# Kernel tuning notes

Hardware: AMD Instinct MI355X
Metric: run time of the kernel (lower is better)

## Reference

```python
import jax, jax.numpy as jnp
import numpy as np

D_MODEL = 1024
N_HEADS = 16
D_K = D_MODEL // N_HEADS
THETA = 10000.0
MAX_SEQ_LEN = 2048


def _rope_tables(seq_len):
    pos = jnp.arange(seq_len, dtype=jnp.float32)
    inv_freq = 1.0 / (THETA ** (jnp.arange(0, D_K, 2, dtype=jnp.float32) / D_K))
    ang = pos[:, None] * inv_freq[None, :]  # [T, D_K/2]
    return jnp.cos(ang), jnp.sin(ang)


def _apply_rope(x, cos, sin):
    # x: [..., T, D_K]; cos/sin: [T, D_K/2]
    x_even = x[..., ::2]
    x_odd = x[..., 1::2]
    r_even = x_even * cos - x_odd * sin
    r_odd = x_even * sin + x_odd * cos
    out = jnp.stack([r_even, r_odd], axis=-1)  # [..., T, D_K/2, 2]
    return out.reshape(x.shape)


def setup_inputs() -> dict:
    key = jax.random.key(0)
    ks = jax.random.split(key, 5)
    std = np.sqrt(2.0 / (D_MODEL + D_MODEL))
    x = jax.random.normal(ks[0], (2, 2048, D_MODEL), dtype=jnp.float32)
    w_q = jax.random.normal(ks[1], (D_MODEL, D_MODEL), dtype=jnp.float32) * std
    w_k = jax.random.normal(ks[2], (D_MODEL, D_MODEL), dtype=jnp.float32) * std
    w_v = jax.random.normal(ks[3], (D_MODEL, D_MODEL), dtype=jnp.float32) * std
    w_o = jax.random.normal(ks[4], (D_MODEL, D_MODEL), dtype=jnp.float32) * std
    return {"x": x, "w_q": w_q, "w_k": w_k, "w_v": w_v, "w_o": w_o}


def reference(x, w_q, w_k, w_v, w_o):
    B, T, _ = x.shape
    # projections: weight stored as [d_out, d_in], y = x @ W^T
    q = jnp.einsum('btd,od->bto', x, w_q)
    k = jnp.einsum('btd,od->bto', x, w_k)
    v = jnp.einsum('btd,od->bto', x, w_v)
    # split heads: [B, T, H*Dk] -> [B, H, T, Dk]
    q = q.reshape(B, T, N_HEADS, D_K).transpose(0, 2, 1, 3)
    k = k.reshape(B, T, N_HEADS, D_K).transpose(0, 2, 1, 3)
    v = v.reshape(B, T, N_HEADS, D_K).transpose(0, 2, 1, 3)
    cos, sin = _rope_tables(T)
    q = _apply_rope(q, cos, sin)
    k = _apply_rope(k, cos, sin)
    scores = jnp.einsum('bhqd,bhkd->bhqk', q, k) / np.sqrt(D_K).astype(np.float32)
    causal = jnp.tril(jnp.ones((T, T), dtype=bool))
    scores = jnp.where(causal, scores, -jnp.inf)
    attn = jax.nn.softmax(scores, axis=-1)
    out = jnp.einsum('bhqk,bhkd->bhqd', attn, v)
    out = out.transpose(0, 2, 1, 3).reshape(B, T, D_MODEL)
    return jnp.einsum('btd,od->bto', out, w_o)
```

## Files before the change

### kernel.cpp

```cpp
#include <hip/hip_runtime.h>
#include <hip/hip_bf16.h>

typedef __bf16 bf16_t;
typedef __bf16 bf16x8 __attribute__((ext_vector_type(8)));
typedef float f32x4 __attribute__((ext_vector_type(4)));
typedef short short4v __attribute__((ext_vector_type(4)));

#define D_MODEL 1024
#define T_SEQ 2048
#define NH 16
#define DKD 64
#define X_ELEMS (4194304u)
#define W_ELEMS (1048576u)
#define Q_SCALE 0.18033688011112042f

__device__ __forceinline__ void async16(const bf16_t* g, bf16_t* l) {
    __builtin_amdgcn_global_load_lds((const __attribute__((address_space(1))) void*)g,
                                     (__attribute__((address_space(3))) void*)l, 16, 0, 0);
}

__global__ __launch_bounds__(256) void convert_kernel(
    const float* __restrict__ x, const float* __restrict__ wq,
    const float* __restrict__ wk, const float* __restrict__ wv,
    const float* __restrict__ wo,
    bf16_t* __restrict__ xb, bf16_t* __restrict__ wqb, bf16_t* __restrict__ wkb,
    bf16_t* __restrict__ wvb, bf16_t* __restrict__ wob)
{
    size_t idx = ((size_t)blockIdx.x * 256 + threadIdx.x) * 4;
    const float* src; bf16_t* dst; size_t off;
    if (idx < X_ELEMS) { src = x; dst = xb; off = idx; }
    else {
        size_t r = idx - X_ELEMS;
        unsigned w = (unsigned)(r >> 20);
        off = r & (W_ELEMS - 1);
        src = (w == 0) ? wq : (w == 1) ? wk : (w == 2) ? wv : wo;
        dst = (w == 0) ? wqb : (w == 1) ? wkb : (w == 2) ? wvb : wob;
    }
    float4 v = *(const float4*)(src + off);
    union { bf16_t b[4]; short4v s; } u;
    u.b[0] = (bf16_t)v.x; u.b[1] = (bf16_t)v.y;
    u.b[2] = (bf16_t)v.z; u.b[3] = (bf16_t)v.w;
    *(short4v*)(dst + off) = u.s;
}

__global__ __launch_bounds__(256) void rope_kernel(float* __restrict__ cost, float* __restrict__ sint)
{
    int idx = blockIdx.x * 256 + threadIdx.x;
    int t = idx >> 5, i = idx & 31;
    float inv = expf(-0.28782313662425572f * (float)i);
    float ang = (float)t * inv;
    float s, c;
    sincosf(ang, &s, &c);
    cost[idx] = c; sint[idx] = s;
}

__global__ __launch_bounds__(256) void gemm_fused(
    const bf16_t* __restrict__ A,
    const bf16_t* __restrict__ W0, const bf16_t* __restrict__ W1, const bf16_t* __restrict__ W2,
    bf16_t* __restrict__ qout, bf16_t* __restrict__ kout, bf16_t* __restrict__ vout,
    const float* __restrict__ cost, const float* __restrict__ sint,
    float* __restrict__ fout, int modeBase)
{
    const int K = 1024;
    __shared__ bf16_t As[128 * 32];
    __shared__ bf16_t Bs[128 * 32];
    const int tid = threadIdx.x;
    const int wave = tid >> 6, lane = tid & 63;
    const int quad = lane >> 4, l16 = lane & 15;
    const int m0 = blockIdx.x * 128;
    const int n0 = blockIdx.y * 128;
    const int wm = (wave >> 1) * 64, wn = (wave & 1) * 64;
    const int mode = modeBase + blockIdx.z;
    const bf16_t* W = (mode == 1) ? W1 : (mode == 2) ? W2 : W0;

    const bf16_t* Afrag = (mode == 2) ? Bs : As;
    const bf16_t* Bfrag = (mode == 2) ? As : Bs;
    const int aoff = (mode == 2) ? wn : wm;
    const int boff = (mode == 2) ? wm : wn;

    const f32x4 fzero = {0.f, 0.f, 0.f, 0.f};
    f32x4 acc[4][4];
    #pragma unroll
    for (int i = 0; i < 4; ++i)
        #pragma unroll
        for (int j = 0; j < 4; ++j) acc[i][j] = fzero;

    for (int k0 = 0; k0 < K; k0 += 32) {
        __syncthreads();
        #pragma unroll
        for (int c = 0; c < 2; ++c) {
            int G = c * 256 + tid;
            int row = G >> 2, go = G & 3;
            async16(A + (size_t)(m0 + row) * K + (k0 + go * 8), As + (size_t)(c * 256 + wave * 64) * 8);
            async16(W + (size_t)(n0 + row) * K + (k0 + go * 8), Bs + (size_t)(c * 256 + wave * 64) * 8);
        }
        __syncthreads();
        bf16x8 af[4], bfv[4];
        #pragma unroll
        for (int mi = 0; mi < 4; ++mi)
            af[mi] = *(const bf16x8*)(Afrag + (aoff + mi * 16 + l16) * 32 + quad * 8);
        #pragma unroll
        for (int ni = 0; ni < 4; ++ni)
            bfv[ni] = *(const bf16x8*)(Bfrag + (boff + ni * 16 + l16) * 32 + quad * 8);
        #pragma unroll
        for (int mi = 0; mi < 4; ++mi)
            #pragma unroll
            for (int ni = 0; ni < 4; ++ni)
                acc[mi][ni] = __builtin_amdgcn_mfma_f32_16x16x32_bf16(af[mi], bfv[ni], acc[mi][ni], 0, 0, 0);
    }

    #pragma unroll
    for (int mi = 0; mi < 4; ++mi) {
        #pragma unroll
        for (int ni = 0; ni < 4; ++ni) {
            #pragma unroll
            for (int reg = 0; reg < 4; ++reg) {
                float v = acc[mi][ni][reg];
                if (mode == 2) {
                    int f   = n0 + wn + mi * 16 + quad * 4 + reg;
                    int tok = m0 + wm + ni * 16 + l16;
                    int t = tok & (T_SEQ - 1), b = tok >> 11;
                    int h = f >> 6, dk = f & 63;
                    vout[(((size_t)b * NH + h) * DKD + dk) * T_SEQ + t] = (bf16_t)v;
                } else {
                    int row = m0 + wm + mi * 16 + quad * 4 + reg;
                    int col = n0 + wn + ni * 16 + l16;
                    if (mode == 3) {
                        fout[(size_t)row * D_MODEL + col] = v;
                    } else {
                        int t = row & (T_SEQ - 1), b = row >> 11;
                        int h = col >> 6, dk = col & 63;
                        float vp = __shfl_xor(v, 1);
                        int fi = dk >> 1;
                        float c = cost[t * 32 + fi], s = sint[t * 32 + fi];
                        float r = (dk & 1) ? (vp * s + v * c) : (v * c - vp * s);
                        if (mode == 0) r *= Q_SCALE;
                        bf16_t* dst = (mode == 0) ? qout : kout;
                        dst[(((size_t)b * NH + h) * T_SEQ + t) * DKD + dk] = (bf16_t)r;
                    }
                }
            }
        }
    }
}

__global__ __launch_bounds__(64, 2) void attn_kernel(
    const bf16_t* __restrict__ Q, const bf16_t* __restrict__ Kb,
    const bf16_t* __restrict__ Vt, bf16_t* __restrict__ O)
{
    __shared__ bf16_t Pw[2][16 * 72];
    const int lane = threadIdx.x;
    const int quad = lane >> 4, l16 = lane & 15;
    const int bh = blockIdx.x;
    const int qw = (63 - (int)blockIdx.y) * 32;

    const bf16_t* kbase = Kb + (size_t)bh * T_SEQ * DKD;
    const bf16_t* vbase = Vt + (size_t)bh * DKD * T_SEQ;

    bf16x8 qf[2][2];
    #pragma unroll
    for (int j = 0; j < 2; ++j) {
        const bf16_t* qp = Q + ((size_t)bh * T_SEQ + qw + j * 16 + l16) * DKD;
        qf[j][0] = *(const bf16x8*)(qp + quad * 8);
        qf[j][1] = *(const bf16x8*)(qp + 32 + quad * 8);
    }
    const f32x4 fzero = {0.f, 0.f, 0.f, 0.f};
    f32x4 oacc[2][4];
    #pragma unroll
    for (int j = 0; j < 2; ++j)
        #pragma unroll
        for (int i = 0; i < 4; ++i) oacc[j][i] = fzero;
    float lsum[2] = {0.f, 0.f};

    const int nkt = (qw + 95) >> 6;

    bf16x8 kcur[4][2], knxt[4][2], vcur[4][2];
    #pragma unroll
    for (int fi = 0; fi < 4; ++fi) {
        const bf16_t* kr = kbase + (size_t)(fi * 16 + l16) * DKD + quad * 8;
        kcur[fi][0] = *(const bf16x8*)(kr);
        kcur[fi][1] = *(const bf16x8*)(kr + 32);
    }

    for (int kt = 0; kt < nkt; ++kt) {
        const int k0 = kt * 64;
        #pragma unroll
        for (int di = 0; di < 4; ++di) {
            const bf16_t* vr = vbase + (size_t)(di * 16 + l16) * T_SEQ + k0 + quad * 8;
            vcur[di][0] = *(const bf16x8*)(vr);
            vcur[di][1] = *(const bf16x8*)(vr + 32);
        }
        if (kt + 1 < nkt) {
            #pragma unroll
            for (int fi = 0; fi < 4; ++fi) {
                const bf16_t* kr = kbase + (size_t)(k0 + 64 + fi * 16 + l16) * DKD + quad * 8;
                knxt[fi][0] = *(const bf16x8*)(kr);
                knxt[fi][1] = *(const bf16x8*)(kr + 32);
            }
        }

        #pragma unroll
        for (int j = 0; j < 2; ++j) {
            if (k0 > qw + j * 16 + 15) continue;
            const int qcol = qw + j * 16 + l16;
            f32x4 s[4];
            #pragma unroll
            for (int fi = 0; fi < 4; ++fi) {
                f32x4 z = fzero;
                z = __builtin_amdgcn_mfma_f32_16x16x32_bf16(kcur[fi][0], qf[j][0], z, 0, 0, 0);
                z = __builtin_amdgcn_mfma_f32_16x16x32_bf16(kcur[fi][1], qf[j][1], z, 0, 0, 0);
                s[fi] = z;
            }
            if (k0 + 63 > qw + j * 16) {
                #pragma unroll
                for (int fi = 0; fi < 4; ++fi)
                    #pragma unroll
                    for (int reg = 0; reg < 4; ++reg) {
                        int key = k0 + fi * 16 + quad * 4 + reg;
                        s[fi][reg] = (key > qcol) ? -__builtin_inff() : s[fi][reg];
                    }
            }
            float sm = 0.f;
            #pragma unroll
            for (int fi = 0; fi < 4; ++fi)
                #pragma unroll
                for (int reg = 0; reg < 4; ++reg) {
                    float p = __builtin_amdgcn_exp2f(s[fi][reg]);
                    s[fi][reg] = p;
                    sm += p;
                }
            lsum[j] += sm;

            bf16_t* pw = &Pw[j][0];
            #pragma unroll
            for (int fi = 0; fi < 4; ++fi) {
                union { bf16_t h[4]; unsigned long long u64; } pk;
                pk.h[0] = (bf16_t)s[fi][0]; pk.h[1] = (bf16_t)s[fi][1];
                pk.h[2] = (bf16_t)s[fi][2]; pk.h[3] = (bf16_t)s[fi][3];
                *(unsigned long long*)(pw + l16 * 72 + fi * 16 + quad * 4) = pk.u64;
            }
            bf16x8 pf[2];
            pf[0] = *(const bf16x8*)(pw + l16 * 72 + quad * 8);
            pf[1] = *(const bf16x8*)(pw + l16 * 72 + 32 + quad * 8);

            #pragma unroll
            for (int di = 0; di < 4; ++di) {
                oacc[j][di] = __builtin_amdgcn_mfma_f32_16x16x32_bf16(vcur[di][0], pf[0], oacc[j][di], 0, 0, 0);
                oacc[j][di] = __builtin_amdgcn_mfma_f32_16x16x32_bf16(vcur[di][1], pf[1], oacc[j][di], 0, 0, 0);
            }
        }

        if (kt + 1 < nkt) {
            #pragma unroll
            for (int fi = 0; fi < 4; ++fi) {
                kcur[fi][0] = knxt[fi][0];
                kcur[fi][1] = knxt[fi][1];
            }
        }
    }

    const int b = bh >> 4, h = bh & 15;
    #pragma unroll
    for (int j = 0; j < 2; ++j) {
        float l = lsum[j];
        l += __shfl_xor(l, 16);
        l += __shfl_xor(l, 32);
        float rl = 1.0f / l;
        int q = qw + j * 16 + l16;
        #pragma unroll
        for (int di = 0; di < 4; ++di) {
            union { bf16_t hh[4]; unsigned long long u64; } ok;
            #pragma unroll
            for (int reg = 0; reg < 4; ++reg) ok.hh[reg] = (bf16_t)(oacc[j][di][reg] * rl);
            int d = di * 16 + quad * 4;
            *(unsigned long long*)(O + ((size_t)b * T_SEQ + q) * D_MODEL + h * DKD + d) = ok.u64;
        }
    }
}

extern "C" void kernel_launch(void* const* d_in, const int* in_sizes, int n_in,
                              void* d_out, int out_size, void* d_ws, size_t ws_size,
                              hipStream_t stream)
{
    const float* x  = (const float*)d_in[0];
    const float* wq = (const float*)d_in[1];
    const float* wk = (const float*)d_in[2];
    const float* wv = (const float*)d_in[3];
    const float* wo = (const float*)d_in[4];
    float* out = (float*)d_out;

    char* ws = (char*)d_ws;
    size_t off = 0;
    auto alloc = [&](size_t bytes) -> void* {
        void* p = ws + off; off += (bytes + 255) & ~(size_t)255; return p;
    };
    bf16_t* xb   = (bf16_t*)alloc((size_t)X_ELEMS * 2);
    bf16_t* wqb  = (bf16_t*)alloc((size_t)W_ELEMS * 2);
    bf16_t* wkb  = (bf16_t*)alloc((size_t)W_ELEMS * 2);
    bf16_t* wvb  = (bf16_t*)alloc((size_t)W_ELEMS * 2);
    bf16_t* wob  = (bf16_t*)alloc((size_t)W_ELEMS * 2);
    bf16_t* qb   = (bf16_t*)alloc((size_t)X_ELEMS * 2);
    bf16_t* kb   = (bf16_t*)alloc((size_t)X_ELEMS * 2);
    bf16_t* vtb  = (bf16_t*)alloc((size_t)X_ELEMS * 2);
    bf16_t* ob   = (bf16_t*)alloc((size_t)X_ELEMS * 2);
    float*  cost = (float*)alloc((size_t)T_SEQ * 32 * 4);
    float*  sint = (float*)alloc((size_t)T_SEQ * 32 * 4);

    convert_kernel<<<8192, 256, 0, stream>>>(x, wq, wk, wv, wo, xb, wqb, wkb, wvb, wob);
    rope_kernel<<<256, 256, 0, stream>>>(cost, sint);
    gemm_fused<<<dim3(32, 8, 3), 256, 0, stream>>>(xb, wqb, wkb, wvb, qb, kb, vtb, cost, sint, nullptr, 0);
    attn_kernel<<<dim3(32, 64), 64, 0, stream>>>(qb, kb, vtb, ob);
    gemm_fused<<<dim3(32, 8, 1), 256, 0, stream>>>(ob, wob, nullptr, nullptr, nullptr, nullptr, nullptr,
                                                   cost, sint, out, 3);
}
```

Measured before the change: 220.2 us.

## Split long causal attention rows across two blocks and replace LDS P transpose with permlane

The attention grid grows from 64 to 96 row-blocks per head. The 32 longest query blocks (upper half of the sequence) are split into two KV chunks, each chunk writes partial fp32 O and row sums to a workspace, and a new combine kernel merges them. This balances the causal triangle across more workgroups. The P matrix is also repacked with v_cvt_pk_bf16 and permlane16_swap instead of going through shared memory, which needs a permuted V load offset, and K double-buffering now swaps register sets instead of copying. The cost is an extra kernel launch and fp32 partial traffic.

```diff
diff --git a/kernel.cpp b/kernel.cpp
--- a/kernel.cpp
+++ b/kernel.cpp
@@ -5,6 +5,7 @@
 typedef __bf16 bf16x8 __attribute__((ext_vector_type(8)));
 typedef float f32x4 __attribute__((ext_vector_type(4)));
 typedef short short4v __attribute__((ext_vector_type(4)));
+typedef unsigned int uint2v __attribute__((ext_vector_type(2)));
 
 #define D_MODEL 1024
 #define T_SEQ 2048
@@ -146,13 +147,18 @@
 
 __global__ __launch_bounds__(64, 2) void attn_kernel(
     const bf16_t* __restrict__ Q, const bf16_t* __restrict__ Kb,
-    const bf16_t* __restrict__ Vt, bf16_t* __restrict__ O)
-{
-    __shared__ bf16_t Pw[2][16 * 72];
+    const bf16_t* __restrict__ Vt, bf16_t* __restrict__ O,
+    float* __restrict__ Opart, float* __restrict__ Lpart)
+{
     const int lane = threadIdx.x;
     const int quad = lane >> 4, l16 = lane & 15;
+    const int vq = (((quad & 1) << 1) | (quad >> 1)) * 8;
     const int bh = blockIdx.x;
-    const int qw = (63 - (int)blockIdx.y) * 32;
+    const int u = blockIdx.y;
+    int y, ktlo, kthi;
+    if (u < 32) { y = u + 32; ktlo = 0; kthi = 16; }
+    else { y = 95 - u; ktlo = (u < 64) ? 16 : 0; kthi = (y * 32 + 95) >> 6; }
+    const int qw = y * 32;
 
     const bf16_t* kbase = Kb + (size_t)bh * T_SEQ * DKD;
     const bf16_t* vbase = Vt + (size_t)bh * DKD * T_SEQ;
@@ -172,110 +178,152 @@
         for (int i = 0; i < 4; ++i) oacc[j][i] = fzero;
     float lsum[2] = {0.f, 0.f};
 
-    const int nkt = (qw + 95) >> 6;
-
-    bf16x8 kcur[4][2], knxt[4][2], vcur[4][2];
+    bf16x8 ka[4][2], kb2[4][2], vcur[4][2];
     #pragma unroll
     for (int fi = 0; fi < 4; ++fi) {
-        const bf16_t* kr = kbase + (size_t)(fi * 16 + l16) * DKD + quad * 8;
-        kcur[fi][0] = *(const bf16x8*)(kr);
-        kcur[fi][1] = *(const bf16x8*)(kr + 32);
-    }
-
-    for (int kt = 0; kt < nkt; ++kt) {
-        const int k0 = kt * 64;
-        #pragma unroll
-        for (int di = 0; di < 4; ++di) {
-            const bf16_t* vr = vbase + (size_t)(di * 16 + l16) * T_SEQ + k0 + quad * 8;
-            vcur[di][0] = *(const bf16x8*)(vr);
-            vcur[di][1] = *(const bf16x8*)(vr + 32);
-        }
-        if (kt + 1 < nkt) {
+        const bf16_t* kr = kbase + (size_t)(ktlo * 64 + fi * 16 + l16) * DKD + quad * 8;
+        ka[fi][0] = *(const bf16x8*)(kr);
+        ka[fi][1] = *(const bf16x8*)(kr + 32);
+    }
+
+#define ATT_TILE(KC, KN) do { \
+    const int k0 = kt * 64; \
+    _Pragma("unroll") \
+    for (int di = 0; di < 4; ++di) { \
+        const bf16_t* vr = vbase + (size_t)(di * 16 + l16) * T_SEQ + k0 + vq; \
+        vcur[di][0] = *(const bf16x8*)(vr); \
+        vcur[di][1] = *(const bf16x8*)(vr + 32); \
+    } \
+    if (kt + 1 < kthi) { \
+        _Pragma("unroll") \
+        for (int fi = 0; fi < 4; ++fi) { \
+            const bf16_t* kr = kbase + (size_t)(k0 + 64 + fi * 16 + l16) * DKD + quad * 8; \
+            KN[fi][0] = *(const bf16x8*)(kr); \
+            KN[fi][1] = *(const bf16x8*)(kr + 32); \
+        } \
+    } \
+    _Pragma("unroll") \
+    for (int j = 0; j < 2; ++j) { \
+        if (k0 > qw + j * 16 + 15) continue;    \
+        const int qcol = qw + j * 16 + l16; \
+        f32x4 s[4]; \
+        _Pragma("unroll") \
+        for (int fi = 0; fi < 4; ++fi) { \
+            f32x4 z = fzero; \
+            z = __builtin_amdgcn_mfma_f32_16x16x32_bf16(KC[fi][0], qf[j][0], z, 0, 0, 0); \
+            z = __builtin_amdgcn_mfma_f32_16x16x32_bf16(KC[fi][1], qf[j][1], z, 0, 0, 0); \
+            s[fi] = z; \
+        } \
+        if (k0 + 63 > qw + j * 16) { \
+            _Pragma("unroll") \
+            for (int fi = 0; fi < 4; ++fi) \
+                _Pragma("unroll") \
+                for (int reg = 0; reg < 4; ++reg) { \
+                    int key = k0 + fi * 16 + quad * 4 + reg; \
+                    s[fi][reg] = (key > qcol) ? -__builtin_inff() : s[fi][reg]; \
+                } \
+        } \
+        float sm = 0.f; \
+        _Pragma("unroll") \
+        for (int fi = 0; fi < 4; ++fi) \
+            _Pragma("unroll") \
+            for (int reg = 0; reg < 4; ++reg) { \
+                float p = __builtin_amdgcn_exp2f(s[fi][reg]); \
+                s[fi][reg] = p; sm += p; \
+            } \
+        lsum[j] += sm; \
+        unsigned wv[4][2]; \
+        _Pragma("unroll") \
+        for (int fi = 0; fi < 4; ++fi) { \
+            asm("v_cvt_pk_bf16_f32 %0, %1, %2" : "=v"(wv[fi][0]) : "v"(s[fi][0]), "v"(s[fi][1])); \
+            asm("v_cvt_pk_bf16_f32 %0, %1, %2" : "=v"(wv[fi][1]) : "v"(s[fi][2]), "v"(s[fi][3])); \
+        } \
+        uint2v r0 = __builtin_amdgcn_permlane16_swap(wv[0][0], wv[1][0], false, false); \
+        uint2v r1 = __builtin_amdgcn_permlane16_swap(wv[0][1], wv[1][1], false, false); \
+        uint2v r2 = __builtin_amdgcn_permlane16_swap(wv[2][0], wv[3][0], false, false); \
+        uint2v r3 = __builtin_amdgcn_permlane16_swap(wv[2][1], wv[3][1], false, false); \
+        union { unsigned uu[4]; bf16x8 v; } p0, p1; \
+        p0.uu[0] = r0[0]; p0.uu[1] = r1[0]; p0.uu[2] = r0[1]; p0.uu[3] = r1[1]; \
+        p1.uu[0] = r2[0]; p1.uu[1] = r3[0]; p1.uu[2] = r2[1]; p1.uu[3] = r3[1]; \
+        _Pragma("unroll") \
+        for (int di = 0; di < 4; ++di) { \
+            oacc[j][di] = __builtin_amdgcn_mfma_f32_16x16x32_bf16(vcur[di][0], p0.v, oacc[j][di], 0, 0, 0); \
+            oacc[j][di] = __builtin_amdgcn_mfma_f32_16x16x32_bf16(vcur[di][1], p1.v, oacc[j][di], 0, 0, 0); \
+        } \
+    } \
+} while (0)
+
+    bool flip = false;
+    for (int kt = ktlo; kt < kthi; ++kt) {
+        if (!flip) { ATT_TILE(ka, kb2); } else { ATT_TILE(kb2, ka); }
+        flip = !flip;
+    }
+#undef ATT_TILE
+
+    if (u >= 64) {
+        const int b = bh >> 4, h = bh & 15;
+        #pragma unroll
+        for (int j = 0; j < 2; ++j) {
+            float l = lsum[j];
+            l += __shfl_xor(l, 16);
+            l += __shfl_xor(l, 32);
+            float rl = 1.0f / l;
+            int q = qw + j * 16 + l16;
             #pragma unroll
-            for (int fi = 0; fi < 4; ++fi) {
-                const bf16_t* kr = kbase + (size_t)(k0 + 64 + fi * 16 + l16) * DKD + quad * 8;
-                knxt[fi][0] = *(const bf16x8*)(kr);
-                knxt[fi][1] = *(const bf16x8*)(kr + 32);
+            for (int di = 0; di < 4; ++di) {
+                union { bf16_t hh[4]; unsigned long long u64; } ok;
+                #pragma unroll
+                for (int reg = 0; reg < 4; ++reg) ok.hh[reg] = (bf16_t)(oacc[j][di][reg] * rl);
+                int d = di * 16 + quad * 4;
+                *(unsigned long long*)(O + ((size_t)b * T_SEQ + q) * D_MODEL + h * DKD + d) = ok.u64;
             }
         }
-
+    } else {
+        const int yy = y - 32;
+        const int chunk = (ktlo == 16) ? 1 : 0;
+        const size_t slot = ((size_t)bh * 32 + yy) * 2 + chunk;
+        float* op = Opart + slot * 2048;
         #pragma unroll
         for (int j = 0; j < 2; ++j) {
-            if (k0 > qw + j * 16 + 15) continue;
-            const int qcol = qw + j * 16 + l16;
-            f32x4 s[4];
+            Lpart[slot * 128 + j * 64 + lane] = lsum[j];
             #pragma unroll
-            for (int fi = 0; fi < 4; ++fi) {
-                f32x4 z = fzero;
-                z = __builtin_amdgcn_mfma_f32_16x16x32_bf16(kcur[fi][0], qf[j][0], z, 0, 0, 0);
-                z = __builtin_amdgcn_mfma_f32_16x16x32_bf16(kcur[fi][1], qf[j][1], z, 0, 0, 0);
-                s[fi] = z;
-            }
-            if (k0 + 63 > qw + j * 16) {
-                #pragma unroll
-                for (int fi = 0; fi < 4; ++fi)
-                    #pragma unroll
-                    for (int reg = 0; reg < 4; ++reg) {
-                        int key = k0 + fi * 16 + quad * 4 + reg;
-                        s[fi][reg] = (key > qcol) ? -__builtin_inff() : s[fi][reg];
-                    }
-            }
-            float sm = 0.f;
-            #pragma unroll
-            for (int fi = 0; fi < 4; ++fi)
-                #pragma unroll
-                for (int reg = 0; reg < 4; ++reg) {
-                    float p = __builtin_amdgcn_exp2f(s[fi][reg]);
-                    s[fi][reg] = p;
-                    sm += p;
-                }
-            lsum[j] += sm;
-
-            bf16_t* pw = &Pw[j][0];
-            #pragma unroll
-            for (int fi = 0; fi < 4; ++fi) {
-                union { bf16_t h[4]; unsigned long long u64; } pk;
-                pk.h[0] = (bf16_t)s[fi][0]; pk.h[1] = (bf16_t)s[fi][1];
-                pk.h[2] = (bf16_t)s[fi][2]; pk.h[3] = (bf16_t)s[fi][3];
-                *(unsigned long long*)(pw + l16 * 72 + fi * 16 + quad * 4) = pk.u64;
-            }
-            bf16x8 pf[2];
-            pf[0] = *(const bf16x8*)(pw + l16 * 72 + quad * 8);
-            pf[1] = *(const bf16x8*)(pw + l16 * 72 + 32 + quad * 8);
-
-            #pragma unroll
-            for (int di = 0; di < 4; ++di) {
-                oacc[j][di] = __builtin_amdgcn_mfma_f32_16x16x32_bf16(vcur[di][0], pf[0], oacc[j][di], 0, 0, 0);
-                oacc[j][di] = __builtin_amdgcn_mfma_f32_16x16x32_bf16(vcur[di][1], pf[1], oacc[j][di], 0, 0, 0);
-            }
+            for (int di = 0; di < 4; ++di)
+                *(f32x4*)(op + ((size_t)(j * 4 + di) * 64 + lane) * 4) = oacc[j][di];
         }
-
-        if (kt + 1 < nkt) {
-            #pragma unroll
-            for (int fi = 0; fi < 4; ++fi) {
-                kcur[fi][0] = knxt[fi][0];
-                kcur[fi][1] = knxt[fi][1];
-            }
-        }
-    }
-
+    }
+}
+
+__global__ __launch_bounds__(256) void combine_kernel(
+    const float* __restrict__ Opart, const float* __restrict__ Lpart, bf16_t* __restrict__ O)
+{
+    const int bh = blockIdx.x, yy = blockIdx.y;
+    const int t = threadIdx.x;
+    const int ql = t >> 3;
+    const int d0 = (t & 7) * 8;
+    const int j = ql >> 4, l16 = ql & 15;
+    const size_t a = (size_t)bh * 32 + yy;
+    const float* A0 = Opart + a * 2 * 2048;
+    const float* A1 = A0 + 2048;
+    const float* L = Lpart + a * 2 * 128 + j * 64 + l16;
+    float l = 0.f;
+    #pragma unroll
+    for (int q = 0; q < 4; ++q) l += L[q * 16] + L[128 + q * 16];
+    const float rl = 1.0f / l;
+    const int di = d0 >> 4;
+    const int quad0 = (d0 & 15) >> 2;
+    union { bf16_t h[8]; bf16x8 v; } ov;
+    #pragma unroll
+    for (int g = 0; g < 2; ++g) {
+        const int off = ((j * 4 + di) * 64 + (quad0 + g) * 16 + l16) * 4;
+        f32x4 x0 = *(const f32x4*)(A0 + off);
+        f32x4 x1 = *(const f32x4*)(A1 + off);
+        #pragma unroll
+        for (int reg = 0; reg < 4; ++reg)
+            ov.h[g * 4 + reg] = (bf16_t)((x0[reg] + x1[reg]) * rl);
+    }
     const int b = bh >> 4, h = bh & 15;
-    #pragma unroll
-    for (int j = 0; j < 2; ++j) {
-        float l = lsum[j];
-        l += __shfl_xor(l, 16);
-        l += __shfl_xor(l, 32);
-        float rl = 1.0f / l;
-        int q = qw + j * 16 + l16;
-        #pragma unroll
-        for (int di = 0; di < 4; ++di) {
-            union { bf16_t hh[4]; unsigned long long u64; } ok;
-            #pragma unroll
-            for (int reg = 0; reg < 4; ++reg) ok.hh[reg] = (bf16_t)(oacc[j][di][reg] * rl);
-            int d = di * 16 + quad * 4;
-            *(unsigned long long*)(O + ((size_t)b * T_SEQ + q) * D_MODEL + h * DKD + d) = ok.u64;
-        }
-    }
+    const int q = 1024 + yy * 32 + ql;
+    *(bf16x8*)(O + ((size_t)b * T_SEQ + q) * D_MODEL + h * DKD + d0) = ov.v;
 }
 
 extern "C" void kernel_launch(void* const* d_in, const int* in_sizes, int n_in,
@@ -305,11 +353,14 @@
     bf16_t* ob   = (bf16_t*)alloc((size_t)X_ELEMS * 2);
     float*  cost = (float*)alloc((size_t)T_SEQ * 32 * 4);
     float*  sint = (float*)alloc((size_t)T_SEQ * 32 * 4);
+    float*  opart = (float*)alloc((size_t)2048 * 2048 * 4);
+    float*  lpart = (float*)alloc((size_t)2048 * 128 * 4);
 
     convert_kernel<<<8192, 256, 0, stream>>>(x, wq, wk, wv, wo, xb, wqb, wkb, wvb, wob);
     rope_kernel<<<256, 256, 0, stream>>>(cost, sint);
     gemm_fused<<<dim3(32, 8, 3), 256, 0, stream>>>(xb, wqb, wkb, wvb, qb, kb, vtb, cost, sint, nullptr, 0);
-    attn_kernel<<<dim3(32, 64), 64, 0, stream>>>(qb, kb, vtb, ob);
+    attn_kernel<<<dim3(32, 96), 64, 0, stream>>>(qb, kb, vtb, ob, opart, lpart);
+    combine_kernel<<<dim3(32, 32), 256, 0, stream>>>(opart, lpart, ob);
     gemm_fused<<<dim3(32, 8, 1), 256, 0, stream>>>(ob, wob, nullptr, nullptr, nullptr, nullptr, nullptr,
                                                    cost, sint, out, 3);
 }
```

After: 222.4 us. No clear change (+1.0%).
